# Kernel tuning notes

Hardware: AMD Instinct MI355X
Metric: run time of the kernel (lower is better)

Reference implementation:

```python
import jax, jax.numpy as jnp
import numpy as np

N_NODES = 50000
N_EDGES = 1600000
HEADS = 6


def _param(key, shape, scale=0.1):
    return scale * jax.random.normal(key, shape, dtype=jnp.float32)


def setup_inputs() -> dict:
    key = jax.random.key(0)
    ks = jax.random.split(key, 20)
    pos = jax.random.normal(ks[0], (N_NODES, 3), dtype=jnp.float32)
    norm = jax.random.normal(ks[1], (N_NODES, 3), dtype=jnp.float32)
    edge_index = jax.random.randint(ks[2], (2, N_EDGES), 0, N_NODES, dtype=jnp.int64)
    # FeaStConv params: weight [in, heads*out], u [in, heads], c [heads], bias [out]
    def conv_params(k, cin, cout):
        k1, k2, k3, k4 = jax.random.split(k, 4)
        return (_param(k1, (cin, HEADS * cout)), _param(k2, (cin, HEADS)),
                _param(k3, (HEADS,)), _param(k4, (cout,)))
    w1, u1, c1, b1 = conv_params(ks[3], 6, 128)
    w2, u2, c2, b2 = conv_params(ks[4], 128, 128)
    w3, u3, c3, b3 = conv_params(ks[5], 128, 128)
    w4, u4, c4, b4 = conv_params(ks[6], 128, 3)
    return {"pos": pos, "norm": norm, "edge_index": edge_index,
            "w1": w1, "u1": u1, "c1": c1, "b1": b1,
            "w2": w2, "u2": u2, "c2": c2, "b2": b2,
            "w3": w3, "u3": u3, "c3": c3, "b3": b3,
            "w4": w4, "u4": u4, "c4": c4, "b4": b4}


def feast_conv(x, edge_index, W, u, c, b, out_channels):
    # FeaStConv (aggr='mean', no self loops):
    #   q_h = softmax_h((x_j - x_i) @ u_h + c_h)
    #   out_i = mean_{j in N(i)} sum_h q_h * (x_j @ W_h) + b
    src, dst = edge_index[0], edge_index[1]
    xj = x[src]                                   # [E, in]
    xi = x[dst]                                   # [E, in]
    q = jax.nn.softmax((xj - xi) @ u + c, axis=-1)  # [E, H]
    xw = (xj @ W).reshape(-1, HEADS, out_channels)  # [E, H, out]
    m = jnp.einsum('ehf,eh->ef', xw, q)            # [E, out]
    n = x.shape[0]
    s = jax.ops.segment_sum(m, dst, num_segments=n)
    cnt = jax.ops.segment_sum(jnp.ones((edge_index.shape[1],), x.dtype), dst,
                              num_segments=n)
    return s / jnp.maximum(cnt, 1.0)[:, None] + b


def reference(pos, norm, edge_index,
              w1, u1, c1, b1, w2, u2, c2, b2,
              w3, u3, c3, b3, w4, u4, c4, b4):
    x = jnp.concatenate([pos, norm], axis=1)      # [N, 6]
    x = jax.nn.relu(feast_conv(x, edge_index, w1, u1, c1, b1, 128))
    x = jax.nn.relu(feast_conv(x, edge_index, w2, u2, c2, b2, 128))
    x = jax.nn.relu(feast_conv(x, edge_index, w3, u3, c3, b3, 128))
    x = feast_conv(x, edge_index, w4, u4, c4, b4, 3)
    return x
```

## Files before the change

### kernel.cpp

```cpp
#include <hip/hip_runtime.h>
#include <hip/hip_bf16.h>


#define HH 6
constexpr int NN = 50000;
constexpr int NE = 1600000;
constexpr int NBK = 196;
constexpr int SWG = 256;
constexpr int EPW = NE / SWG;

typedef __attribute__((ext_vector_type(8))) short bf16x8;
typedef __attribute__((ext_vector_type(4))) float f32x4;

static __device__ __forceinline__ float b2f(__hip_bfloat16 v) { return __bfloat162float(v); }
static __device__ __forceinline__ float u2f(unsigned short u) {
    return __uint_as_float(((unsigned int)u) << 16);
}
static __device__ __forceinline__ unsigned short f2bu(float v) {
    __hip_bfloat16 b = __float2bfloat16(v);
    return *reinterpret_cast<unsigned short*>(&b);
}
static __device__ __forceinline__ float lo2f(unsigned int w) {
    return __uint_as_float(w << 16);
}
static __device__ __forceinline__ float hi2f(unsigned int w) {
    return __uint_as_float(w & 0xffff0000u);
}
static __device__ __forceinline__ unsigned int pk2(float lo, float hi) {
    return ((unsigned int)f2bu(hi) << 16) | (unsigned int)f2bu(lo);
}
static __device__ __forceinline__ float ldf(const void* p, int i, int f32) {
    return f32 ? ((const float*)p)[i] : b2f(((const __hip_bfloat16*)p)[i]);
}
static __device__ __forceinline__ int ldi(const int* e32, int i, int i64) {
    return i64 ? e32[2 * i] : e32[i];
}
static __device__ __forceinline__ void dma4(const void* g, void* l) {
    __builtin_amdgcn_global_load_lds(
        (const __attribute__((address_space(1))) void*)g,
        (__attribute__((address_space(3))) void*)l, 4, 0, 0);
}

__global__ void k_detect(const void* pos, const void* ei, int* flags) {
    __shared__ float smax[256];
    __shared__ int anynz;
    int t = threadIdx.x;
    if (t == 0) anynz = 0;
    const __hip_bfloat16* pb = (const __hip_bfloat16*)pos;
    float m = 0.f;
    for (int i = t; i < 2048; i += 256) {
        float v = fabsf(b2f(pb[i]));
        if (v != v) v = 1e30f;
        m = fmaxf(m, v);
    }
    smax[t] = m;
    __syncthreads();
    for (int s = 128; s > 0; s >>= 1) {
        if (t < s) smax[t] = fmaxf(smax[t], smax[t + s]);
        __syncthreads();
    }
    const int* e32 = (const int*)ei;
    if (t < 128 && e32[2 * t + 1] != 0) anynz = 1;
    __syncthreads();
    if (t == 0) {
        flags[0] = (smax[0] > 1e6f) ? 1 : 0;
        flags[1] = anynz ? 0 : 1;
    }
}

__global__ void k_build_x0(const void* __restrict__ pos, const void* __restrict__ nrm,
                           const void* __restrict__ u1,
                           unsigned short* __restrict__ x0b, float* __restrict__ p8,
                           const int* __restrict__ flags) {
    int f32 = flags[0];
    int i = blockIdx.x * blockDim.x + threadIdx.x;
    if (i >= NN) return;
    float xv[6];
#pragma unroll
    for (int j = 0; j < 3; j++) {
        unsigned short a = f32 ? f2bu(((const float*)pos)[i * 3 + j])
                               : ((const unsigned short*)pos)[i * 3 + j];
        unsigned short b = f32 ? f2bu(((const float*)nrm)[i * 3 + j])
                               : ((const unsigned short*)nrm)[i * 3 + j];
        x0b[i * 8 + j]     = a;
        x0b[i * 8 + 3 + j] = b;
        xv[j]     = u2f(a);
        xv[3 + j] = u2f(b);
    }
    x0b[i * 8 + 6] = 0;
    x0b[i * 8 + 7] = 0;
    float acc[HH] = {};
#pragma unroll
    for (int k = 0; k < 6; k++)
#pragma unroll
        for (int h = 0; h < HH; h++) acc[h] = fmaf(xv[k], ldf(u1, k * HH + h, f32), acc[h]);
#pragma unroll
    for (int h = 0; h < HH; h++) p8[(size_t)i * 8 + h] = acc[h];
    p8[(size_t)i * 8 + 6] = 0.f;
    p8[(size_t)i * 8 + 7] = 0.f;
}

__global__ void __launch_bounds__(256) k_sortA(const int* __restrict__ ei,
                                               int* __restrict__ cntT,
                                               const int* __restrict__ flags) {
    __shared__ int hist[NBK];
    int i64 = flags[1];
    int t = threadIdx.x, w = blockIdx.x;
    for (int b = t; b < NBK; b += 256) hist[b] = 0;
    __syncthreads();
    int start = w * EPW, end = start + EPW;
    for (int e = start + t; e < end; e += 256) {
        int d = ldi(ei, NE + e, i64);
        atomicAdd(&hist[d >> 8], 1);
    }
    __syncthreads();
    for (int b = t; b < NBK; b += 256) cntT[b * SWG + w] = hist[b];
}

__global__ void __launch_bounds__(256) k_scan_local(const int* __restrict__ a, int n,
                                                    int* __restrict__ o,
                                                    int* __restrict__ bsums) {
    __shared__ int ws[4];
    int b = blockIdx.x, t = threadIdx.x, lane = t & 63, wid = t >> 6;
    int idx = b * 256 + t;
    int v = (idx < n) ? a[idx] : 0;
    int incl = v;
#pragma unroll
    for (int off = 1; off < 64; off <<= 1) {
        int nb = __shfl_up(incl, off, 64);
        if (lane >= off) incl += nb;
    }
    if (lane == 63) ws[wid] = incl;
    __syncthreads();
    int wpre = 0, tot = 0;
#pragma unroll
    for (int wi = 0; wi < 4; wi++) {
        int s = ws[wi];
        if (wi < wid) wpre += s;
        tot += s;
    }
    if (idx < n) o[idx] = wpre + incl - v;
    if (t == 0) bsums[b] = tot;
}

__global__ void __launch_bounds__(256) k_scan_sums(const int* __restrict__ bsums,
                                                   int* __restrict__ bpre,
                                                   int* __restrict__ o, int n, int nb) {
    __shared__ int ws[4];
    int t = threadIdx.x, lane = t & 63, wid = t >> 6;
    int v = (t < nb) ? bsums[t] : 0;
    int incl = v;
#pragma unroll
    for (int off = 1; off < 64; off <<= 1) {
        int nbv = __shfl_up(incl, off, 64);
        if (lane >= off) incl += nbv;
    }
    if (lane == 63) ws[wid] = incl;
    __syncthreads();
    int wpre = 0, tot = 0;
#pragma unroll
    for (int wi = 0; wi < 4; wi++) {
        int s = ws[wi];
        if (wi < wid) wpre += s;
        tot += s;
    }
    if (t < nb) bpre[t] = wpre + incl - v;
    if (t == 0) o[n] = tot;
}

__global__ void __launch_bounds__(256) k_scan_add(int* __restrict__ o, int n,
                                                  const int* __restrict__ bpre) {
    int idx = blockIdx.x * 256 + threadIdx.x;
    if (idx < n) o[idx] += bpre[blockIdx.x];
}

__global__ void __launch_bounds__(256) k_sortB(const int* __restrict__ ei,
                                               const int* __restrict__ base2,
                                               unsigned int* __restrict__ ebuck,
                                               const int* __restrict__ flags) {
    __shared__ int cur[NBK];
    int i64 = flags[1];
    int t = threadIdx.x, w = blockIdx.x;
    for (int b = t; b < NBK; b += 256) cur[b] = base2[b * SWG + w];
    __syncthreads();
    int start = w * EPW, end = start + EPW;
    for (int e = start + t; e < end; e += 256) {
        int s = ldi(ei, e, i64), d = ldi(ei, NE + e, i64);
        int slot = atomicAdd(&cur[d >> 8], 1);
        ebuck[slot] = (unsigned int)s | ((unsigned int)(d & 255) << 16);
    }
}

__global__ void __launch_bounds__(256) k_sortC(const unsigned int* __restrict__ ebuck,
                                               const int* __restrict__ base2,
                                               int* __restrict__ offs,
                                               int* __restrict__ ssrc) {
    __shared__ int cnt[256];
    __shared__ int ws[4];
    int t = threadIdx.x, b = blockIdx.x;
    int lane = t & 63, wid = t >> 6;
    cnt[t] = 0;
    __syncthreads();
    int bs = base2[b * SWG], be = base2[(b + 1) * SWG];
    for (int e = bs + t; e < be; e += 256)
        atomicAdd(&cnt[(ebuck[e] >> 16) & 255], 1);
    __syncthreads();
    int v = cnt[t];
    int incl = v;
#pragma unroll
    for (int off = 1; off < 64; off <<= 1) {
        int nb = __shfl_up(incl, off, 64);
        if (lane >= off) incl += nb;
    }
    if (lane == 63) ws[wid] = incl;
    __syncthreads();
    int wpre = 0;
#pragma unroll
    for (int wi = 0; wi < 4; wi++)
        if (wi < wid) wpre += ws[wi];
    int excl = wpre + incl - v;
    int gn = b * 256 + t;
    if (gn <= NN) offs[gn] = bs + excl;
    __syncthreads();
    cnt[t] = bs + excl;
    __syncthreads();
    for (int e = bs + t; e < be; e += 256) {
        unsigned int rec = ebuck[e];
        int slot = atomicAdd(&cnt[(rec >> 16) & 255], 1);
        ssrc[slot] = (int)(rec & 0xffffu);
    }
}

__global__ void __launch_bounds__(256) k_compute_p128(const unsigned short* __restrict__ x,
                                                      const void* __restrict__ u,
                                                      float* __restrict__ p8,
                                                      const int* __restrict__ flags) {
    int f32 = flags[0];
    int wave = (blockIdx.x * blockDim.x + threadIdx.x) >> 6;
    int lane = threadIdx.x & 63;
    if (wave >= NN) return;
    unsigned int w = *(const unsigned int*)(x + (size_t)wave * 128 + 2 * lane);
    float x0 = lo2f(w);
    float x1 = hi2f(w);
    float acc[HH];
#pragma unroll
    for (int h = 0; h < HH; h++)
        acc[h] = x0 * ldf(u, (2 * lane) * HH + h, f32) + x1 * ldf(u, (2 * lane + 1) * HH + h, f32);
#pragma unroll
    for (int off = 32; off > 0; off >>= 1) {
#pragma unroll
        for (int h = 0; h < HH; h++) acc[h] += __shfl_down(acc[h], off, 64);
    }
    if (lane == 0) {
#pragma unroll
        for (int h = 0; h < HH; h++) p8[(size_t)wave * 8 + h] = acc[h];
    }
}

__global__ void __launch_bounds__(256) k_agg128(const unsigned short* __restrict__ xb,
                                                const float* __restrict__ p8,
                                                const void* __restrict__ cvec,
                                                const int* __restrict__ ssrc,
                                                const int* __restrict__ offs,
                                                unsigned short* __restrict__ agg,
                                                const int* __restrict__ flags) {
    __shared__ float qs[4][64][8];
    int f32 = flags[0];
    int wid = threadIdx.x >> 6, lane = threadIdx.x & 63;
    int node = (blockIdx.x * blockDim.x + threadIdx.x) >> 6;
    if (node >= NN) return;
    int s0 = offs[node], s1 = offs[node + 1];
    int deg = s1 - s0;
    float scale = 1.0f / (float)(deg > 0 ? deg : 1);
    const float* pn = p8 + (size_t)node * 8;
    float pd[HH];
#pragma unroll
    for (int h = 0; h < HH; h++) pd[h] = pn[h] - ldf(cvec, h, f32);

    float a0[HH] = {}, a1[HH] = {};
    for (int base = s0; base < s1; base += 64) {
        int cnt = (s1 - base < 64) ? (s1 - base) : 64;
        unsigned int rowElem = 0;
        {
            int e = base + lane;
            float q0 = 0, q1 = 0, q2 = 0, q3 = 0, q4 = 0, q5 = 0;
            if (e < s1) {
                int j = ssrc[e];
                const float* pj = p8 + (size_t)j * 8;
                float4 pa = *(const float4*)pj;
                float2 pb = *(const float2*)(pj + 4);
                float t0 = pa.x - pd[0], t1 = pa.y - pd[1], t2 = pa.z - pd[2];
                float t3 = pa.w - pd[3], t4 = pb.x - pd[4], t5 = pb.y - pd[5];
                float mx = fmaxf(fmaxf(fmaxf(t0, t1), fmaxf(t2, t3)), fmaxf(t4, t5));
                q0 = __expf(t0 - mx); q1 = __expf(t1 - mx); q2 = __expf(t2 - mx);
                q3 = __expf(t3 - mx); q4 = __expf(t4 - mx); q5 = __expf(t5 - mx);
                float inv = 1.0f / (q0 + q1 + q2 + q3 + q4 + q5);
                q0 *= inv; q1 *= inv; q2 *= inv; q3 *= inv; q4 *= inv; q5 *= inv;
                rowElem = (unsigned int)j * 128u;
            }
            float4 qa = {q0, q1, q2, q3};
            float2 qb = {q4, q5};
            *(float4*)&qs[wid][lane][0] = qa;
            *(float2*)&qs[wid][lane][4] = qb;
        }
        int cnt8 = (cnt + 7) & ~7;
        for (int s = 0; s < cnt8; s += 8) {
            unsigned int xw[8];
#pragma unroll
            for (int u = 0; u < 8; u++) {
                unsigned int ro =
                    (unsigned int)__builtin_amdgcn_readlane((int)rowElem, s + u);
                xw[u] = *(const unsigned int*)(xb + (size_t)ro + 2 * lane);
            }
#pragma unroll
            for (int u = 0; u < 8; u++) {
                float4 qa = *(const float4*)&qs[wid][s + u][0];
                float2 qb = *(const float2*)&qs[wid][s + u][4];
                float x0v = lo2f(xw[u]);
                float x1v = hi2f(xw[u]);
                a0[0] = fmaf(qa.x, x0v, a0[0]);
                a1[0] = fmaf(qa.x, x1v, a1[0]);
                a0[1] = fmaf(qa.y, x0v, a0[1]);
                a1[1] = fmaf(qa.y, x1v, a1[1]);
                a0[2] = fmaf(qa.z, x0v, a0[2]);
                a1[2] = fmaf(qa.z, x1v, a1[2]);
                a0[3] = fmaf(qa.w, x0v, a0[3]);
                a1[3] = fmaf(qa.w, x1v, a1[3]);
                a0[4] = fmaf(qb.x, x0v, a0[4]);
                a1[4] = fmaf(qb.x, x1v, a1[4]);
                a0[5] = fmaf(qb.y, x0v, a0[5]);
                a1[5] = fmaf(qb.y, x1v, a1[5]);
            }
        }
    }
    unsigned short* ar = agg + (size_t)node * 768;
#pragma unroll
    for (int h = 0; h < HH; h++) {
        *(unsigned int*)(ar + h * 128 + 2 * lane) = pk2(a0[h] * scale, a1[h] * scale);
    }
}

__global__ void __launch_bounds__(256) k_agg6(const unsigned short* __restrict__ xb,
                                              const float* __restrict__ p8,
                                              const void* __restrict__ cvec,
                                              const int* __restrict__ ssrc,
                                              const int* __restrict__ offs,
                                              float* __restrict__ agg,
                                              const int* __restrict__ flags) {
    __shared__ unsigned short stage6[4][64 * 8];
    __shared__ float qsf[4][64][8];
    int f32 = flags[0];
    int wid = threadIdx.x >> 6, lane = threadIdx.x & 63;
    int node = (blockIdx.x * blockDim.x + threadIdx.x) >> 6;
    if (node >= NN) return;
    int s0 = offs[node], s1 = offs[node + 1];
    int deg = s1 - s0;
    float scale = 1.0f / (float)(deg > 0 ? deg : 1);
    const float* pn = p8 + (size_t)node * 8;
    float pd[HH];
#pragma unroll
    for (int h = 0; h < HH; h++) pd[h] = pn[h] - ldf(cvec, h, f32);

    float acc6 = 0.f;
    int hh6 = lane / 6, kk6 = lane - hh6 * 6;
    const char* xbase = (const char*)xb;
    for (int base = s0; base < s1; base += 64) {
        int cnt = (s1 - base < 64) ? (s1 - base) : 64;
        {
            int e = base + lane;
            float q0 = 0, q1 = 0, q2 = 0, q3 = 0, q4 = 0, q5 = 0;
            unsigned int rowByte = 0;
            if (e < s1) {
                int j = ssrc[e];
                const float* pj = p8 + (size_t)j * 8;
                float4 pa = *(const float4*)pj;
                float2 pb = *(const float2*)(pj + 4);
                float t0 = pa.x - pd[0], t1 = pa.y - pd[1], t2 = pa.z - pd[2];
                float t3 = pa.w - pd[3], t4 = pb.x - pd[4], t5 = pb.y - pd[5];
                float mx = fmaxf(fmaxf(fmaxf(t0, t1), fmaxf(t2, t3)), fmaxf(t4, t5));
                q0 = __expf(t0 - mx); q1 = __expf(t1 - mx); q2 = __expf(t2 - mx);
                q3 = __expf(t3 - mx); q4 = __expf(t4 - mx); q5 = __expf(t5 - mx);
                float inv = 1.0f / (q0 + q1 + q2 + q3 + q4 + q5);
                q0 *= inv; q1 *= inv; q2 *= inv; q3 *= inv; q4 *= inv; q5 *= inv;
                rowByte = (unsigned int)j * 16u;
            }
            float4 qa = {q0, q1, q2, q3};
            float4 qb = {q4, q5, __uint_as_float(rowByte), 0.f};
            *(float4*)&qsf[wid][lane][0] = qa;
            *(float4*)&qsf[wid][lane][4] = qb;
        }
        __builtin_amdgcn_sched_barrier(0);
#pragma unroll
        for (int t = 0; t < 4; t++) {
            int r = t * 16 + (lane >> 2);
            unsigned int rb = __float_as_uint(qsf[wid][r][6]);
            dma4(xbase + rb + (lane & 3) * 4, &stage6[wid][t * 128]);
        }
        __builtin_amdgcn_s_waitcnt(0x0f70);
        __builtin_amdgcn_sched_barrier(0);
        if (lane < 36) {
            for (int s = 0; s < cnt; s++) {
                float qh = qsf[wid][s][hh6];
                float xv = u2f(stage6[wid][s * 8 + kk6]);
                acc6 = fmaf(qh, xv, acc6);
            }
        }
        __builtin_amdgcn_sched_barrier(0);
    }
    if (lane < 36) agg[(size_t)node * 36 + lane] = acc6 * scale;
}

__global__ void k_repack_all(const void* __restrict__ W1, const void* __restrict__ W2,
                             const void* __restrict__ W3, const void* __restrict__ W4,
                             const void* __restrict__ U4,
                             float* __restrict__ wstk1, unsigned short* __restrict__ wt2,
                             unsigned short* __restrict__ wt3, unsigned short* __restrict__ wt4,
                             unsigned short* __restrict__ u4,
                             const int* __restrict__ flags) {
    int f32 = flags[0];
    int idx = blockIdx.x * blockDim.x + threadIdx.x;
    if (idx < 4608) {
        int f = idx & 127, m = idx >> 7;
        int h = m / 6, k = m - h * 6;
        wstk1[idx] = ldf(W1, k * 768 + h * 128 + f, f32);
        return;
    }
    idx -= 4608;
    if (idx < 98304) {
        int f = idx / 768, m = idx % 768;
        int h = m >> 7, kk = m & 127;
        wt2[idx] = f2bu(ldf(W2, kk * 768 + h * 128 + f, f32));
        return;
    }
    idx -= 98304;
    if (idx < 98304) {
        int f = idx / 768, m = idx % 768;
        int h = m >> 7, kk = m & 127;
        wt3[idx] = f2bu(ldf(W3, kk * 768 + h * 128 + f, f32));
        return;
    }
    idx -= 98304;
    if (idx < 4096) {
        int n = idx >> 7, k = idx & 127;
        wt4[idx] = (n < 18) ? f2bu(ldf(W4, k * 18 + n, f32)) : (unsigned short)0;
        return;
    }
    idx -= 4096;
    if (idx < 2048) {
        int n = idx >> 7, k = idx & 127;
        u4[idx] = (n < 6) ? f2bu(ldf(U4, k * 6 + n, f32)) : (unsigned short)0;
    }
}

__global__ void __launch_bounds__(256) k_gemm_f32(const float* __restrict__ A,
                                                  const float* __restrict__ B,
                                                  const void* __restrict__ bias,
                                                  unsigned short* __restrict__ C,
                                                  int M, int K, int relu,
                                                  const int* __restrict__ flags) {
    int f32 = flags[0];
    __shared__ float As[16][68];
    __shared__ float Bs[16][128];
    int tid = threadIdx.x;
    int tx = tid & 15;
    int ty = tid >> 4;
    int bm = blockIdx.x * 64;
    int arow = tid >> 2, ak = (tid & 3) * 4;
    int brow = tid >> 4, bcol = (tid & 15) * 8;
    float acc[4][8] = {};
    for (int k0 = 0; k0 < K; k0 += 16) {
        float4 av = {0, 0, 0, 0};
        int gr = bm + arow;
        if (gr < M && (k0 + ak) < K) av = *(const float4*)(A + (size_t)gr * K + k0 + ak);
        As[ak + 0][arow] = av.x;
        As[ak + 1][arow] = av.y;
        As[ak + 2][arow] = av.z;
        As[ak + 3][arow] = av.w;
        float4 bv0 = {0, 0, 0, 0}, bv1 = {0, 0, 0, 0};
        if ((k0 + brow) < K) {
            const float* bp = B + (size_t)(k0 + brow) * 128 + bcol;
            bv0 = *(const float4*)bp;
            bv1 = *(const float4*)(bp + 4);
        }
        *(float4*)&Bs[brow][bcol]     = bv0;
        *(float4*)&Bs[brow][bcol + 4] = bv1;
        __syncthreads();
#pragma unroll
        for (int kk = 0; kk < 16; kk++) {
            float a_[4], b_[8];
#pragma unroll
            for (int j = 0; j < 4; j++) a_[j] = As[kk][ty * 4 + j];
#pragma unroll
            for (int j = 0; j < 8; j++) b_[j] = Bs[kk][tx * 8 + j];
#pragma unroll
            for (int i = 0; i < 4; i++)
#pragma unroll
                for (int j = 0; j < 8; j++) acc[i][j] = fmaf(a_[i], b_[j], acc[i][j]);
        }
        __syncthreads();
    }
#pragma unroll
    for (int i = 0; i < 4; i++) {
        int row = bm + ty * 4 + i;
        if (row >= M) continue;
#pragma unroll
        for (int j = 0; j < 8; j++) {
            int col = tx * 8 + j;
            float v = acc[i][j] + ldf(bias, col, f32);
            if (relu) v = fmaxf(v, 0.f);
            C[(size_t)row * 128 + col] = f2bu(v);
        }
    }
}

__global__ void __launch_bounds__(256) k_gemm_mfma(const unsigned short* __restrict__ A,
                                                   const unsigned short* __restrict__ Bt,
                                                   const void* __restrict__ bias,
                                                   unsigned short* __restrict__ C,
                                                   int M, int relu,
                                                   const int* __restrict__ flags) {
    constexpr int K = 768, BK = 64;
    __shared__ unsigned short As[64][72];
    __shared__ unsigned short Bs[128][72];
    int f32 = flags[0];
    int tid = threadIdx.x;
    int lane = tid & 63, wid = tid >> 6;
    int wm = wid & 1, wn = wid >> 1;
    int bm = blockIdx.x * 64;
    int l15 = lane & 15, lq = lane >> 4;
    f32x4 acc[2][4] = {};

    for (int k0 = 0; k0 < K; k0 += BK) {
#pragma unroll
        for (int cc = 0; cc < 2; cc++) {
            int c = tid + cc * 256;
            int r = c >> 3, kc = (c & 7) * 8;
            bf16x8 av = {};
            int gr = bm + r;
            if (gr < M) av = *(const bf16x8*)(A + (size_t)gr * K + k0 + kc);
            *(bf16x8*)&As[r][kc] = av;
        }
#pragma unroll
        for (int cc = 0; cc < 4; cc++) {
            int c = tid + cc * 256;
            int n = c >> 3, kc = (c & 7) * 8;
            *(bf16x8*)&Bs[n][kc] = *(const bf16x8*)(Bt + (size_t)n * K + k0 + kc);
        }
        __syncthreads();
#pragma unroll
        for (int ks = 0; ks < BK; ks += 32) {
            int koff = ks + lq * 8;
            bf16x8 af[2], bfr[4];
#pragma unroll
            for (int tm = 0; tm < 2; tm++)
                af[tm] = *(const bf16x8*)&As[wm * 32 + tm * 16 + l15][koff];
#pragma unroll
            for (int tn = 0; tn < 4; tn++)
                bfr[tn] = *(const bf16x8*)&Bs[wn * 64 + tn * 16 + l15][koff];
#pragma unroll
            for (int tm = 0; tm < 2; tm++)
#pragma unroll
                for (int tn = 0; tn < 4; tn++)
                    acc[tm][tn] = __builtin_amdgcn_mfma_f32_16x16x32_bf16(
                        af[tm], bfr[tn], acc[tm][tn], 0, 0, 0);
        }
        __syncthreads();
    }
#pragma unroll
    for (int tm = 0; tm < 2; tm++) {
#pragma unroll
        for (int tn = 0; tn < 4; tn++) {
            int col = wn * 64 + tn * 16 + l15;
            float bv = ldf(bias, col, f32);
#pragma unroll
            for (int r = 0; r < 4; r++) {
                int row = bm + wm * 32 + tm * 16 + lq * 4 + r;
                if (row < M) {
                    float v = acc[tm][tn][r] + bv;
                    if (relu) v = fmaxf(v, 0.f);
                    C[(size_t)row * 128 + col] = f2bu(v);
                }
            }
        }
    }
}

__global__ void __launch_bounds__(256) k_y4p(const unsigned short* __restrict__ xb,
                                             const unsigned short* __restrict__ wt4,
                                             const unsigned short* __restrict__ u4,
                                             unsigned short* __restrict__ y4h,
                                             float* __restrict__ p8) {
    int tid = threadIdx.x;
    int lane = tid & 63, wid = tid >> 6;
    int l15 = lane & 15, lq = lane >> 4;
    int bm = blockIdx.x * 64 + wid * 16;
    f32x4 acc[2] = {};
    f32x4 accp = {};
#pragma unroll
    for (int ks = 0; ks < 128; ks += 32) {
        int koff = ks + lq * 8;
        bf16x8 af = {};
        int row = bm + l15;
        if (row < NN) af = *(const bf16x8*)(xb + (size_t)row * 128 + koff);
        bf16x8 b0 = *(const bf16x8*)(wt4 + (0 * 16 + l15) * 128 + koff);
        bf16x8 b1 = *(const bf16x8*)(wt4 + (1 * 16 + l15) * 128 + koff);
        bf16x8 bu = *(const bf16x8*)(u4 + l15 * 128 + koff);
        acc[0] = __builtin_amdgcn_mfma_f32_16x16x32_bf16(af, b0, acc[0], 0, 0, 0);
        acc[1] = __builtin_amdgcn_mfma_f32_16x16x32_bf16(af, b1, acc[1], 0, 0, 0);
        accp = __builtin_amdgcn_mfma_f32_16x16x32_bf16(af, bu, accp, 0, 0, 0);
    }
#pragma unroll
    for (int t = 0; t < 2; t++) {
#pragma unroll
        for (int r = 0; r < 4; r++) {
            int row = bm + lq * 4 + r;
            int col = t * 16 + l15;
            if (row < NN && col < 18) y4h[(size_t)row * 24 + col] = f2bu(acc[t][r]);
        }
    }
#pragma unroll
    for (int r = 0; r < 4; r++) {
        int row = bm + lq * 4 + r;
        if (row < NN && l15 < 6) p8[(size_t)row * 8 + l15] = accp[r];
    }
}

__global__ void __launch_bounds__(256) k_final_fast(const unsigned short* __restrict__ y4h,
                                                    const float* __restrict__ p8,
                                                    const void* __restrict__ cvec,
                                                    const int* __restrict__ ssrc,
                                                    const int* __restrict__ offs,
                                                    const void* __restrict__ bias,
                                                    void* __restrict__ out,
                                                    const int* __restrict__ flags) {
    int f32 = flags[0];
    int lane = threadIdx.x & 63;
    int node = (blockIdx.x * blockDim.x + threadIdx.x) >> 6;
    if (node >= NN) return;
    int s0 = offs[node], s1 = offs[node + 1];
    int deg = s1 - s0;
    float scale = 1.0f / (float)(deg > 0 ? deg : 1);
    const float* pn = p8 + (size_t)node * 8;
    float pd[HH];
#pragma unroll
    for (int h = 0; h < HH; h++) pd[h] = pn[h] - ldf(cvec, h, f32);

    float f0 = 0, f1 = 0, f2 = 0;
    for (int base = s0; base < s1; base += 64) {
        int e = base + lane;
        if (e < s1) {
            int j = ssrc[e];
            const float* pj = p8 + (size_t)j * 8;
            float4 pa = *(const float4*)pj;
            float2 pb = *(const float2*)(pj + 4);
            float t0 = pa.x - pd[0], t1 = pa.y - pd[1], t2 = pa.z - pd[2];
            float t3 = pa.w - pd[3], t4 = pb.x - pd[4], t5 = pb.y - pd[5];
            float mx = fmaxf(fmaxf(fmaxf(t0, t1), fmaxf(t2, t3)), fmaxf(t4, t5));
            float q0 = __expf(t0 - mx), q1 = __expf(t1 - mx), q2 = __expf(t2 - mx);
            float q3 = __expf(t3 - mx), q4 = __expf(t4 - mx), q5 = __expf(t5 - mx);
            float inv = 1.0f / (q0 + q1 + q2 + q3 + q4 + q5);
            float qa[6] = {q0 * inv, q1 * inv, q2 * inv, q3 * inv, q4 * inv, q5 * inv};
            const unsigned int* yr = (const unsigned int*)(y4h + (size_t)j * 24);
            uint4 ua = *(const uint4*)yr;
            uint4 ub = *(const uint4*)(yr + 4);
            unsigned int uc = yr[8];
            unsigned int d[9] = {ua.x, ua.y, ua.z, ua.w, ub.x, ub.y, ub.z, ub.w, uc};
            float yv[18];
#pragma unroll
            for (int c = 0; c < 18; c++)
                yv[c] = (c & 1) ? hi2f(d[c >> 1]) : lo2f(d[c >> 1]);
#pragma unroll
            for (int h = 0; h < HH; h++) {
                f0 = fmaf(qa[h], yv[3 * h + 0], f0);
                f1 = fmaf(qa[h], yv[3 * h + 1], f1);
                f2 = fmaf(qa[h], yv[3 * h + 2], f2);
            }
        }
    }
#pragma unroll
    for (int off = 32; off > 0; off >>= 1) {
        f0 += __shfl_down(f0, off, 64);
        f1 += __shfl_down(f1, off, 64);
        f2 += __shfl_down(f2, off, 64);
    }
    if (lane == 0) {
        float r0 = f0 * scale + ldf(bias, 0, f32);
        float r1 = f1 * scale + ldf(bias, 1, f32);
        float r2 = f2 * scale + ldf(bias, 2, f32);
        if (f32) {
            float* o = (float*)out;
            o[(size_t)node * 3 + 0] = r0;
            o[(size_t)node * 3 + 1] = r1;
            o[(size_t)node * 3 + 2] = r2;
        } else {
            __hip_bfloat16* o = (__hip_bfloat16*)out;
            o[(size_t)node * 3 + 0] = __float2bfloat16(r0);
            o[(size_t)node * 3 + 1] = __float2bfloat16(r1);
            o[(size_t)node * 3 + 2] = __float2bfloat16(r2);
        }
    }
}

extern "C" void kernel_launch(void* const* d_in, const int* in_sizes, int n_in,
                              void* d_out, int out_size, void* d_ws, size_t ws_size,
                              hipStream_t stream) {
    (void)in_sizes; (void)n_in; (void)out_size; (void)ws_size;
    const void* pos = d_in[0];
    const void* nrm = d_in[1];
    const int* ei = (const int*)d_in[2];
    const void* W[4] = {d_in[3], d_in[7], d_in[11], d_in[15]};
    const void* U[4] = {d_in[4], d_in[8], d_in[12], d_in[16]};
    const void* Cc[4] = {d_in[5], d_in[9], d_in[13], d_in[17]};
    const void* Bb[4] = {d_in[6], d_in[10], d_in[14], d_in[18]};

    char* wp = (char*)d_ws;
    auto alloc = [&](size_t b) { void* r = (void*)wp; wp += (b + 255) & ~(size_t)255; return r; };
    unsigned short* xA  = (unsigned short*)alloc((size_t)NN * 128 * 2);
    unsigned short* xB  = (unsigned short*)alloc((size_t)NN * 128 * 2);
    unsigned short* x0b = (unsigned short*)alloc((size_t)NN * 8 * 2);
    float* p8     = (float*)alloc((size_t)NN * 8 * 4);
    unsigned short* y4h = (unsigned short*)alloc((size_t)NN * 24 * 2);
    int*   offs   = (int*)alloc((size_t)(NN + 1) * 4);
    int*   cntT   = (int*)alloc((size_t)NBK * SWG * 4);
    int*   base2  = (int*)alloc((size_t)(NBK * SWG + 1) * 4);
    int*   bsums  = (int*)alloc((size_t)256 * 4);
    int*   bpre   = (int*)alloc((size_t)256 * 4);
    int*   flags  = (int*)alloc(256);
    int*   ssrc   = (int*)alloc((size_t)NE * 4);
    unsigned int* ebuck = (unsigned int*)alloc((size_t)NE * 4);
    void*  aggv   = alloc((size_t)NN * 768 * 2);
    float* wstk1  = (float*)alloc((size_t)36 * 128 * 4);
    unsigned short* wt2 = (unsigned short*)alloc((size_t)128 * 768 * 2);
    unsigned short* wt3 = (unsigned short*)alloc((size_t)128 * 768 * 2);
    unsigned short* wt4 = (unsigned short*)alloc((size_t)32 * 128 * 2);
    unsigned short* u4  = (unsigned short*)alloc((size_t)16 * 128 * 2);
    unsigned short* agg_h = (unsigned short*)aggv;
    float* agg_f = (float*)aggv;

    const int NB = (NN + 255) / 256;
    const int NWB = (NN * 64 + 255) / 256;
    const int GB = (NN + 63) / 64;
    const int NSC = NBK * SWG;

    k_detect<<<1, 256, 0, stream>>>(pos, ei, flags);
    k_sortA<<<SWG, 256, 0, stream>>>(ei, cntT, flags);
    k_scan_local<<<NBK, 256, 0, stream>>>(cntT, NSC, base2, bsums);
    k_scan_sums<<<1, 256, 0, stream>>>(bsums, bpre, base2, NSC, NBK);
    k_scan_add<<<NBK, 256, 0, stream>>>(base2, NSC, bpre);
    k_sortB<<<SWG, 256, 0, stream>>>(ei, base2, ebuck, flags);
    k_sortC<<<NBK, 256, 0, stream>>>(ebuck, base2, offs, ssrc);
    k_build_x0<<<NB, 256, 0, stream>>>(pos, nrm, U[0], x0b, p8, flags);
    k_repack_all<<<(207360 + 255) / 256, 256, 0, stream>>>(W[0], W[1], W[2], W[3], U[3],
                                                           wstk1, wt2, wt3, wt4, u4, flags);

    k_agg6<<<NWB, 256, 0, stream>>>(x0b, p8, Cc[0], ssrc, offs, agg_f, flags);
    k_gemm_f32<<<GB, 256, 0, stream>>>(agg_f, wstk1, Bb[0], xA, NN, 36, 1, flags);

    k_compute_p128<<<NWB, 256, 0, stream>>>(xA, U[1], p8, flags);
    k_agg128<<<NWB, 256, 0, stream>>>(xA, p8, Cc[1], ssrc, offs, agg_h, flags);
    k_gemm_mfma<<<GB, 256, 0, stream>>>(agg_h, wt2, Bb[1], xB, NN, 1, flags);

    k_compute_p128<<<NWB, 256, 0, stream>>>(xB, U[2], p8, flags);
    k_agg128<<<NWB, 256, 0, stream>>>(xB, p8, Cc[2], ssrc, offs, agg_h, flags);
    k_gemm_mfma<<<GB, 256, 0, stream>>>(agg_h, wt3, Bb[2], xA, NN, 1, flags);

    k_y4p<<<GB, 256, 0, stream>>>(xA, wt4, u4, y4h, p8);
    k_final_fast<<<NWB, 256, 0, stream>>>(y4h, p8, Cc[3], ssrc, offs, Bb[3], d_out, flags);
}
```

Measured before the change: 544.7 us.

## Fuse per-node attention projection into GEMM epilogues, drop compute_p128 kernels

Removes the two standalone k_compute_p128 launches and instead computes p = x·U for the next layer inside the epilogues of k_gemm_f32 and k_gemm_mfma, using the bf16-rounded outputs already in registers. U2/U3 are repacked to fp32 in k_repack_all, and partial sums are reduced with shuffles and then with shared-memory atomics in the MFMA kernel. The goal is to avoid re-reading the 128-wide activations and to save two kernel launches, at the cost of extra epilogue work, register pressure and an extra block barrier in the GEMMs. The zeroing of p8 columns 6 and 7 is also removed.

```diff
diff --git a/kernel.cpp b/kernel.cpp
--- a/kernel.cpp
+++ b/kernel.cpp
@@ -96,8 +96,6 @@
         for (int h = 0; h < HH; h++) acc[h] = fmaf(xv[k], ldf(u1, k * HH + h, f32), acc[h]);
 #pragma unroll
     for (int h = 0; h < HH; h++) p8[(size_t)i * 8 + h] = acc[h];
-    p8[(size_t)i * 8 + 6] = 0.f;
-    p8[(size_t)i * 8 + 7] = 0.f;
 }
 
 __global__ void __launch_bounds__(256) k_sortA(const int* __restrict__ ei,
@@ -228,32 +226,6 @@
         unsigned int rec = ebuck[e];
         int slot = atomicAdd(&cnt[(rec >> 16) & 255], 1);
         ssrc[slot] = (int)(rec & 0xffffu);
-    }
-}
-
-__global__ void __launch_bounds__(256) k_compute_p128(const unsigned short* __restrict__ x,
-                                                      const void* __restrict__ u,
-                                                      float* __restrict__ p8,
-                                                      const int* __restrict__ flags) {
-    int f32 = flags[0];
-    int wave = (blockIdx.x * blockDim.x + threadIdx.x) >> 6;
-    int lane = threadIdx.x & 63;
-    if (wave >= NN) return;
-    unsigned int w = *(const unsigned int*)(x + (size_t)wave * 128 + 2 * lane);
-    float x0 = lo2f(w);
-    float x1 = hi2f(w);
-    float acc[HH];
-#pragma unroll
-    for (int h = 0; h < HH; h++)
-        acc[h] = x0 * ldf(u, (2 * lane) * HH + h, f32) + x1 * ldf(u, (2 * lane + 1) * HH + h, f32);
-#pragma unroll
-    for (int off = 32; off > 0; off >>= 1) {
-#pragma unroll
-        for (int h = 0; h < HH; h++) acc[h] += __shfl_down(acc[h], off, 64);
-    }
-    if (lane == 0) {
-#pragma unroll
-        for (int h = 0; h < HH; h++) p8[(size_t)wave * 8 + h] = acc[h];
     }
 }
 
@@ -412,10 +384,12 @@
 
 __global__ void k_repack_all(const void* __restrict__ W1, const void* __restrict__ W2,
                              const void* __restrict__ W3, const void* __restrict__ W4,
+                             const void* __restrict__ U2, const void* __restrict__ U3,
                              const void* __restrict__ U4,
                              float* __restrict__ wstk1, unsigned short* __restrict__ wt2,
                              unsigned short* __restrict__ wt3, unsigned short* __restrict__ wt4,
                              unsigned short* __restrict__ u4,
+                             float* __restrict__ uf2, float* __restrict__ uf3,
                              const int* __restrict__ flags) {
     int f32 = flags[0];
     int idx = blockIdx.x * blockDim.x + threadIdx.x;
@@ -449,13 +423,25 @@
     if (idx < 2048) {
         int n = idx >> 7, k = idx & 127;
         u4[idx] = (n < 6) ? f2bu(ldf(U4, k * 6 + n, f32)) : (unsigned short)0;
+        return;
+    }
+    idx -= 2048;
+    if (idx < 768) {
+        uf2[idx] = ldf(U2, idx, f32);
+        return;
+    }
+    idx -= 768;
+    if (idx < 768) {
+        uf3[idx] = ldf(U3, idx, f32);
     }
 }
 
 __global__ void __launch_bounds__(256) k_gemm_f32(const float* __restrict__ A,
                                                   const float* __restrict__ B,
                                                   const void* __restrict__ bias,
+                                                  const float* __restrict__ uf,
                                                   unsigned short* __restrict__ C,
+                                                  float* __restrict__ p8,
                                                   int M, int K, int relu,
                                                   const int* __restrict__ flags) {
     int f32 = flags[0];
@@ -502,13 +488,44 @@
 #pragma unroll
     for (int i = 0; i < 4; i++) {
         int row = bm + ty * 4 + i;
-        if (row >= M) continue;
 #pragma unroll
         for (int j = 0; j < 8; j++) {
             int col = tx * 8 + j;
             float v = acc[i][j] + ldf(bias, col, f32);
             if (relu) v = fmaxf(v, 0.f);
-            C[(size_t)row * 128 + col] = f2bu(v);
+            unsigned short hv = f2bu(v);
+            if (row < M) C[(size_t)row * 128 + col] = hv;
+            acc[i][j] = u2f(hv);
+        }
+    }
+    float uu[8][HH];
+#pragma unroll
+    for (int j = 0; j < 8; j++) {
+        int col = tx * 8 + j;
+#pragma unroll
+        for (int h = 0; h < HH; h++) uu[j][h] = uf[col * HH + h];
+    }
+    float pp[4][HH] = {};
+#pragma unroll
+    for (int i = 0; i < 4; i++)
+#pragma unroll
+        for (int j = 0; j < 8; j++)
+#pragma unroll
+            for (int h = 0; h < HH; h++) pp[i][h] = fmaf(acc[i][j], uu[j][h], pp[i][h]);
+#pragma unroll
+    for (int m = 1; m < 16; m <<= 1)
+#pragma unroll
+        for (int i = 0; i < 4; i++)
+#pragma unroll
+            for (int h = 0; h < HH; h++) pp[i][h] += __shfl_xor(pp[i][h], m, 64);
+    if (tx == 0) {
+#pragma unroll
+        for (int i = 0; i < 4; i++) {
+            int row = bm + ty * 4 + i;
+            if (row < M) {
+#pragma unroll
+                for (int h = 0; h < HH; h++) p8[(size_t)row * 8 + h] = pp[i][h];
+            }
         }
     }
 }
@@ -516,7 +533,9 @@
 __global__ void __launch_bounds__(256) k_gemm_mfma(const unsigned short* __restrict__ A,
                                                    const unsigned short* __restrict__ Bt,
                                                    const void* __restrict__ bias,
+                                                   const float* __restrict__ uf,
                                                    unsigned short* __restrict__ C,
+                                                   float* __restrict__ p8,
                                                    int M, int relu,
                                                    const int* __restrict__ flags) {
     constexpr int K = 768, BK = 64;
@@ -575,12 +594,57 @@
 #pragma unroll
             for (int r = 0; r < 4; r++) {
                 int row = bm + wm * 32 + tm * 16 + lq * 4 + r;
-                if (row < M) {
-                    float v = acc[tm][tn][r] + bv;
-                    if (relu) v = fmaxf(v, 0.f);
-                    C[(size_t)row * 128 + col] = f2bu(v);
+                float v = acc[tm][tn][r] + bv;
+                if (relu) v = fmaxf(v, 0.f);
+                unsigned short hv = f2bu(v);
+                if (row < M) C[(size_t)row * 128 + col] = hv;
+                acc[tm][tn][r] = u2f(hv);
+            }
+        }
+    }
+    if (p8) {
+        float* pl = (float*)&As[0][0];
+        if (tid < 384) pl[tid] = 0.f;
+        float uu[4][HH];
+#pragma unroll
+        for (int tn = 0; tn < 4; tn++) {
+            int col = wn * 64 + tn * 16 + l15;
+#pragma unroll
+            for (int h = 0; h < HH; h++) uu[tn][h] = uf[col * HH + h];
+        }
+        __syncthreads();
+#pragma unroll
+        for (int tm = 0; tm < 2; tm++) {
+            float pp[4][HH] = {};
+#pragma unroll
+            for (int tn = 0; tn < 4; tn++)
+#pragma unroll
+                for (int r = 0; r < 4; r++)
+#pragma unroll
+                    for (int h = 0; h < HH; h++)
+                        pp[r][h] = fmaf(acc[tm][tn][r], uu[tn][h], pp[r][h]);
+#pragma unroll
+            for (int m = 1; m < 16; m <<= 1)
+#pragma unroll
+                for (int r = 0; r < 4; r++)
+#pragma unroll
+                    for (int h = 0; h < HH; h++)
+                        pp[r][h] += __shfl_xor(pp[r][h], m, 64);
+            if (l15 == 0) {
+#pragma unroll
+                for (int r = 0; r < 4; r++) {
+                    int lrow = wm * 32 + tm * 16 + lq * 4 + r;
+#pragma unroll
+                    for (int h = 0; h < HH; h++)
+                        atomicAdd(&pl[lrow * HH + h], pp[r][h]);
                 }
             }
+        }
+        __syncthreads();
+        if (tid < 384) {
+            int lrow = tid / 6;
+            int grow = bm + lrow;
+            if (grow < M) p8[(size_t)grow * 8 + (tid - lrow * 6)] = pl[tid];
         }
     }
 }
@@ -734,6 +798,8 @@
     unsigned short* wt3 = (unsigned short*)alloc((size_t)128 * 768 * 2);
     unsigned short* wt4 = (unsigned short*)alloc((size_t)32 * 128 * 2);
     unsigned short* u4  = (unsigned short*)alloc((size_t)16 * 128 * 2);
+    float* uf2    = (float*)alloc((size_t)768 * 4);
+    float* uf3    = (float*)alloc((size_t)768 * 4);
     unsigned short* agg_h = (unsigned short*)aggv;
     float* agg_f = (float*)aggv;
 
@@ -750,19 +816,19 @@
     k_sortB<<<SWG, 256, 0, stream>>>(ei, base2, ebuck, flags);
     k_sortC<<<NBK, 256, 0, stream>>>(ebuck, base2, offs, ssrc);
     k_build_x0<<<NB, 256, 0, stream>>>(pos, nrm, U[0], x0b, p8, flags);
-    k_repack_all<<<(207360 + 255) / 256, 256, 0, stream>>>(W[0], W[1], W[2], W[3], U[3],
-                                                           wstk1, wt2, wt3, wt4, u4, flags);
+    k_repack_all<<<(208896 + 255) / 256, 256, 0, stream>>>(W[0], W[1], W[2], W[3],
+                                                           U[1], U[2], U[3],
+                                                           wstk1, wt2, wt3, wt4, u4,
+                                                           uf2, uf3, flags);
 
     k_agg6<<<NWB, 256, 0, stream>>>(x0b, p8, Cc[0], ssrc, offs, agg_f, flags);
-    k_gemm_f32<<<GB, 256, 0, stream>>>(agg_f, wstk1, Bb[0], xA, NN, 36, 1, flags);
-
-    k_compute_p128<<<NWB, 256, 0, stream>>>(xA, U[1], p8, flags);
+    k_gemm_f32<<<GB, 256, 0, stream>>>(agg_f, wstk1, Bb[0], uf2, xA, p8, NN, 36, 1, flags);
+
     k_agg128<<<NWB, 256, 0, stream>>>(xA, p8, Cc[1], ssrc, offs, agg_h, flags);
-    k_gemm_mfma<<<GB, 256, 0, stream>>>(agg_h, wt2, Bb[1], xB, NN, 1, flags);
-
-    k_compute_p128<<<NWB, 256, 0, stream>>>(xB, U[2], p8, flags);
+    k_gemm_mfma<<<GB, 256, 0, stream>>>(agg_h, wt2, Bb[1], uf3, xB, p8, NN, 1, flags);
+
     k_agg128<<<NWB, 256, 0, stream>>>(xB, p8, Cc[2], ssrc, offs, agg_h, flags);
-    k_gemm_mfma<<<GB, 256, 0, stream>>>(agg_h, wt3, Bb[2], xA, NN, 1, flags);
+    k_gemm_mfma<<<GB, 256, 0, stream>>>(agg_h, wt3, Bb[2], nullptr, xA, nullptr, NN, 1, flags);
 
     k_y4p<<<GB, 256, 0, stream>>>(xA, wt4, u4, y4h, p8);
     k_final_fast<<<NWB, 256, 0, stream>>>(y4h, p8, Cc[3], ssrc, offs, Bb[3], d_out, flags);
```

Measured after the change: 478.9 us. -12.1%, faster.
